# Performance work log

Measured on AMD Instinct MI355X. Metric: run time of the kernel, lower is better.

The kernel has to match this reference:

```python
import jax, jax.numpy as jnp
import numpy as np

D_MODEL = 1024
NUM_HEADS = 16


def setup_inputs() -> dict:
    key = jax.random.key(0)
    ks = jax.random.split(key, 5)
    sigma = (2.0 / (D_MODEL + D_MODEL)) ** 0.5
    def trunc(k):
        # truncated normal in [-3*sigma, 3*sigma], std sigma
        return sigma * jax.random.truncated_normal(k, -3.0, 3.0, (D_MODEL, D_MODEL), jnp.float32)
    x = jax.random.normal(ks[0], (4, 2048, D_MODEL), jnp.float32)
    return {
        "x": x,
        "W_Q": trunc(ks[1]),
        "W_K": trunc(ks[2]),
        "W_V": trunc(ks[3]),
        "W_O": trunc(ks[4]),
    }


def _mha(x, W_Q, W_K, W_V, W_O):
    B, S, D = x.shape
    H = NUM_HEADS
    dk = D // H
    # Linear stores W as (d_out, d_in); einsum '... d_in, d_out d_in -> ... d_out'
    Q = jnp.einsum('bsd,ed->bse', x, W_Q).reshape(B, S, H, dk).transpose(0, 2, 1, 3)
    K = jnp.einsum('bsd,ed->bse', x, W_K).reshape(B, S, H, dk).transpose(0, 2, 1, 3)
    V = jnp.einsum('bsd,ed->bse', x, W_V).reshape(B, S, H, dk).transpose(0, 2, 1, 3)
    scores = jnp.einsum('bhnd,bhmd->bhnm', Q, K) / jnp.sqrt(jnp.asarray(dk, x.dtype))
    causal = jnp.tril(jnp.ones((S, S), bool))
    scores = jnp.where(causal, scores, -jnp.inf)
    attn = jax.nn.softmax(scores, axis=-1)
    out = jnp.einsum('bhnm,bhmd->bhnd', attn, V)  # [B,H,S,dk]
    out = out.transpose(0, 2, 1, 3).reshape(B, S, D)
    return jnp.einsum('bsd,ed->bse', out, W_O)


def reference(x, W_Q, W_K, W_V, W_O):
    return _mha(x, W_Q, W_K, W_V, W_O)
```

## Files before the change

### kernel.cpp

```cpp
#include <hip/hip_runtime.h>
#include <hip/hip_bf16.h>
#include <stdint.h>


typedef unsigned short u16;
typedef short bf16x8 __attribute__((ext_vector_type(8)));
typedef float f32x4 __attribute__((ext_vector_type(4)));
typedef unsigned short u16x8 __attribute__((ext_vector_type(8)));
typedef unsigned int u32x4 __attribute__((ext_vector_type(4)));

#define S_LEN 2048
#define DMODEL 1024
#define NH 16

__device__ __forceinline__ u16 f2bf(float f) {
    unsigned u = __builtin_bit_cast(unsigned, f);
    unsigned r = (u + 0x7fffu + ((u >> 16) & 1u)) >> 16;
    return (u16)r;
}

__device__ __forceinline__ float fast_exp2(float x) {
    return __builtin_amdgcn_exp2f(x);
}

__device__ __forceinline__ unsigned cvtpk_bf16(float lo, float hi_) {
    unsigned r;
    asm("v_cvt_pk_bf16_f32 %0, %1, %2" : "=v"(r) : "v"(lo), "v"(hi_));
    return r;
}

__device__ __forceinline__ void pl32swap(unsigned& a, unsigned& b) {
    asm("v_permlane32_swap_b32 %0, %1" : "+v"(a), "+v"(b));
}
__device__ __forceinline__ void pl16swap(unsigned& a, unsigned& b) {
    asm("v_permlane16_swap_b32 %0, %1" : "+v"(a), "+v"(b));
}

__device__ __forceinline__ void gll16(const void* g, void* s) {
    __builtin_amdgcn_global_load_lds((const __attribute__((address_space(1))) unsigned*)g,
                                     (__attribute__((address_space(3))) unsigned*)s, 16, 0, 0);
}

__global__ __launch_bounds__(256) void cast_all(
    const float* __restrict__ x, const float* __restrict__ wq, const float* __restrict__ wk,
    const float* __restrict__ wv, const float* __restrict__ wo,
    u16* __restrict__ xb, u16* __restrict__ wqkv, u16* __restrict__ wob, int nx) {
    const int NW = DMODEL * DMODEL;
    int i4 = (blockIdx.x * 256 + threadIdx.x) * 4;
    const float* src; u16* dst; int off;
    if (i4 < nx)             { src = x;  dst = xb;            off = i4; }
    else if (i4 < nx + NW)   { src = wq; dst = wqkv;          off = i4 - nx; }
    else if (i4 < nx + 2*NW) { src = wk; dst = wqkv + NW;     off = i4 - nx - NW; }
    else if (i4 < nx + 3*NW) { src = wv; dst = wqkv + 2*NW;   off = i4 - nx - 2*NW; }
    else                     { src = wo; dst = wob;           off = i4 - nx - 3*NW; }
    float4 v = *reinterpret_cast<const float4*>(src + off);
    ushort4 o4; o4.x = f2bf(v.x); o4.y = f2bf(v.y); o4.z = f2bf(v.z); o4.w = f2bf(v.w);
    *reinterpret_cast<ushort4*>(dst + off) = o4;
}

template <typename OUT>
__global__ __launch_bounds__(256) void gemm_bt(const u16* __restrict__ A, const u16* __restrict__ B,
                                               OUT* __restrict__ C, int M, int N, int K,
                                               int qcols, float qscale, u16* __restrict__ vt) {
    __shared__ u16 As[128 * 64];
    __shared__ u16 Bs[128 * 64];
    __shared__ u16 Ts[4][16 * 72];
    const int m0 = blockIdx.y * 128, n0 = blockIdx.x * 128;
    const int t = threadIdx.x, w = t >> 6, l = t & 63;
    const int hi = l >> 4;
    const int wr = w >> 1, wc = w & 1;
    f32x4 acc[4][4] = {};

    const int lr = l >> 3;
    const int lc = l & 7;
    const int gcol = (lc ^ lr) * 8;
    const u16* Ag = A + (size_t)(m0 + w * 32 + lr) * K + gcol;
    const u16* Bg = B + (size_t)(n0 + w * 32 + lr) * K + gcol;

    for (int k0 = 0; k0 < K; k0 += 64) {
        __syncthreads();
#pragma unroll
        for (int c = 0; c < 4; c++) {
            gll16(Ag + (size_t)c * 8 * K + k0, As + w * 2048 + c * 512);
            gll16(Bg + (size_t)c * 8 * K + k0, Bs + w * 2048 + c * 512);
        }
        __syncthreads();
#pragma unroll
        for (int kk = 0; kk < 2; kk++) {
            bf16x8 af[4], bfr[4];
#pragma unroll
            for (int mi = 0; mi < 4; mi++)
                af[mi] = *(const bf16x8*)&As[(wr * 64 + mi * 16 + (l & 15)) * 64 +
                                             (((kk * 4 + hi) ^ (l & 7)) * 8)];
#pragma unroll
            for (int ni = 0; ni < 4; ni++)
                bfr[ni] = *(const bf16x8*)&Bs[(wc * 64 + ni * 16 + (l & 15)) * 64 +
                                              (((kk * 4 + hi) ^ (l & 7)) * 8)];
#pragma unroll
            for (int mi = 0; mi < 4; mi++)
#pragma unroll
                for (int ni = 0; ni < 4; ni++)
                    acc[mi][ni] = __builtin_amdgcn_mfma_f32_16x16x32_bf16(af[mi], bfr[ni], acc[mi][ni], 0, 0, 0);
        }
    }

    if (vt != nullptr && n0 >= 2048) {
        const int mw = m0 + wr * 64;
        const int bq = mw >> 11;
        const int s0w = mw & (S_LEN - 1);
        const int hd = ((n0 + wc * 64) - 2048) >> 6;
        u16* tb = &Ts[w][0];
#pragma unroll
        for (int ni = 0; ni < 4; ni++) {
#pragma unroll
            for (int mi = 0; mi < 4; mi++) {
                uint2 pk = make_uint2(cvtpk_bf16(acc[mi][ni][0], acc[mi][ni][1]),
                                      cvtpk_bf16(acc[mi][ni][2], acc[mi][ni][3]));
                *(uint2*)&tb[(l & 15) * 72 + mi * 16 + hi * 4] = pk;
            }
            bf16x8 r0 = *(const bf16x8*)&tb[(l & 15) * 72 + hi * 16];
            bf16x8 r1 = *(const bf16x8*)&tb[(l & 15) * 72 + hi * 16 + 8];
            size_t vrow = ((size_t)(bq * 16 + hd) * 64 + ni * 16 + (l & 15)) * S_LEN + s0w + hi * 16;
            *(u16x8*)&vt[vrow]     = (u16x8)r0;
            *(u16x8*)&vt[vrow + 8] = (u16x8)r1;
        }
    } else {
#pragma unroll
        for (int mi = 0; mi < 4; mi++)
#pragma unroll
            for (int ni = 0; ni < 4; ni++)
#pragma unroll
                for (int j = 0; j < 4; j++) {
                    int r = m0 + wr * 64 + mi * 16 + hi * 4 + j;
                    int c = n0 + wc * 64 + ni * 16 + (l & 15);
                    float v = acc[mi][ni][j];
                    if (c < qcols) v *= qscale;
                    if constexpr (__is_same(OUT, u16)) C[(size_t)r * N + c] = f2bf(v);
                    else                               C[(size_t)r * N + c] = v;
                }
    }
}

__global__ __launch_bounds__(256, 3) void attn(const u16* __restrict__ QKV, const u16* __restrict__ VT,
                                               u16* __restrict__ O) {
    const int bh = blockIdx.x, y = blockIdx.y;
    const int p = (y < 8) ? y : 23 - y;
    const int b = bh >> 4, h = bh & 15;
    const int t = threadIdx.x, w = t >> 6, l = t & 63;
    const int q = l & 15, hi = l >> 4, s7 = q & 7;

    __shared__ u16 SM[2][2][64][64];

    const int srow = t >> 3, sblk = t & 7;
    const int gs = (sblk ^ (srow & 7)) * 8;
    const u16* Kg = QKV + (size_t)(b * S_LEN + srow) * 3072 + 1024 + h * 64 + gs;
    const u16* Vg = VT + (size_t)(bh * 64 + srow) * S_LEN + gs;
    const u16* Kg2 = Kg + (size_t)32 * 3072;
    const u16* Vg2 = Vg + (size_t)32 * S_LEN;

    const int kA0 = q * 128 + ((hi ^ s7) << 4);
    const int kA1 = kA0 ^ 64;
    const char* smbase = (const char*)&SM[0][0][0][0];

    const int q128 = p * 128;
    const int nt = 2 * p + 2;
    const int qgA = q128 + w * 16 + q;
    const int qgB = qgA + 64;

    bf16x8 qfA[2], qfB[2];
#pragma unroll
    for (int kk = 0; kk < 2; kk++) {
        qfA[kk] = *(const bf16x8*)&QKV[(size_t)(b * S_LEN + qgA) * 3072 + h * 64 + kk * 32 + hi * 8];
        qfB[kk] = *(const bf16x8*)&QKV[(size_t)(b * S_LEN + qgB) * 3072 + h * 64 + kk * 32 + hi * 8];
    }

    f32x4 oaccA[4] = {}, oaccB[4] = {};
    float ssA = 0.f, ssB = 0.f;

    gll16(Kg,  (u16*)&SM[0][0][0][0] + t * 8);
    gll16(Kg2, (u16*)&SM[0][0][0][0] + 2048 + t * 8);
    gll16(Vg,  (u16*)&SM[0][1][0][0] + t * 8);
    gll16(Vg2, (u16*)&SM[0][1][0][0] + 2048 + t * 8);
    __syncthreads();

    const u16* KgT  = Kg  + (size_t)64 * 3072;
    const u16* Kg2T = Kg2 + (size_t)64 * 3072;
    const u16* VgT  = Vg  + 64;
    const u16* Vg2T = Vg2 + 64;

#pragma unroll 1
    for (int tt = 0; tt < nt; ++tt) {
        const int cur = tt & 1;
        if (tt + 1 < nt) {
            gll16(KgT,  (u16*)&SM[cur ^ 1][0][0][0] + t * 8);
            gll16(Kg2T, (u16*)&SM[cur ^ 1][0][0][0] + 2048 + t * 8);
            gll16(VgT,  (u16*)&SM[cur ^ 1][1][0][0] + t * 8);
            gll16(Vg2T, (u16*)&SM[cur ^ 1][1][0][0] + 2048 + t * 8);
            KgT  += (size_t)64 * 3072;
            Kg2T += (size_t)64 * 3072;
            VgT  += 64;
            Vg2T += 64;
        }
        const int kv0 = tt * 64;
        const char* kb = smbase + cur * 16384;

        f32x4 saccA[4] = {}, saccB[4] = {};
        __builtin_amdgcn_s_setprio(1);
#pragma unroll
        for (int kk = 0; kk < 2; kk++) {
            const char* ka = kb + (kk ? kA1 : kA0);
#pragma unroll
            for (int ni = 0; ni < 4; ni++) {
                bf16x8 kf = *(const bf16x8*)(ka + ni * 2048);
                saccA[ni] = __builtin_amdgcn_mfma_f32_16x16x32_bf16(kf, qfA[kk], saccA[ni], 0, 0, 0);
                saccB[ni] = __builtin_amdgcn_mfma_f32_16x16x32_bf16(kf, qfB[kk], saccB[ni], 0, 0, 0);
            }
        }
        __builtin_amdgcn_s_setprio(0);

        bf16x8 pfA0, pfA1, pfB0, pfB1;
        {
            const int r0 = qgA - kv0;
            if (r0 < 63) {
                const int rth = r0 - hi * 4;
#pragma unroll
                for (int ni = 0; ni < 4; ni++)
#pragma unroll
                    for (int j = 0; j < 4; j++)
                        if (ni * 16 + j > rth) saccA[ni][j] = -1e30f;
            }
            float pv[4][4];
#pragma unroll
            for (int ni = 0; ni < 4; ni++)
#pragma unroll
                for (int j = 0; j < 4; j++) pv[ni][j] = fast_exp2(saccA[ni][j] - 8.0f);
            ssA += ((pv[0][0] + pv[0][1]) + (pv[0][2] + pv[0][3]))
                 + ((pv[1][0] + pv[1][1]) + (pv[1][2] + pv[1][3]))
                 + ((pv[2][0] + pv[2][1]) + (pv[2][2] + pv[2][3]))
                 + ((pv[3][0] + pv[3][1]) + (pv[3][2] + pv[3][3]));
            unsigned c00 = cvtpk_bf16(pv[0][0], pv[0][1]), c01 = cvtpk_bf16(pv[0][2], pv[0][3]);
            unsigned c10 = cvtpk_bf16(pv[1][0], pv[1][1]), c11 = cvtpk_bf16(pv[1][2], pv[1][3]);
            unsigned c20 = cvtpk_bf16(pv[2][0], pv[2][1]), c21 = cvtpk_bf16(pv[2][2], pv[2][3]);
            unsigned c30 = cvtpk_bf16(pv[3][0], pv[3][1]), c31 = cvtpk_bf16(pv[3][2], pv[3][3]);
            pl32swap(c00, c10); pl16swap(c00, c10);
            pl32swap(c01, c11); pl16swap(c01, c11);
            pl32swap(c20, c30); pl16swap(c20, c30);
            pl32swap(c21, c31); pl16swap(c21, c31);
            u32x4 f0 = {c00, c01, c10, c11};
            u32x4 f1 = {c20, c21, c30, c31};
            pfA0 = __builtin_bit_cast(bf16x8, f0);
            pfA1 = __builtin_bit_cast(bf16x8, f1);
        }
        {
            const int r0 = qgB - kv0;
            if (r0 < 63) {
                const int rth = r0 - hi * 4;
#pragma unroll
                for (int ni = 0; ni < 4; ni++)
#pragma unroll
                    for (int j = 0; j < 4; j++)
                        if (ni * 16 + j > rth) saccB[ni][j] = -1e30f;
            }
            float pv[4][4];
#pragma unroll
            for (int ni = 0; ni < 4; ni++)
#pragma unroll
                for (int j = 0; j < 4; j++) pv[ni][j] = fast_exp2(saccB[ni][j] - 8.0f);
            ssB += ((pv[0][0] + pv[0][1]) + (pv[0][2] + pv[0][3]))
                 + ((pv[1][0] + pv[1][1]) + (pv[1][2] + pv[1][3]))
                 + ((pv[2][0] + pv[2][1]) + (pv[2][2] + pv[2][3]))
                 + ((pv[3][0] + pv[3][1]) + (pv[3][2] + pv[3][3]));
            unsigned c00 = cvtpk_bf16(pv[0][0], pv[0][1]), c01 = cvtpk_bf16(pv[0][2], pv[0][3]);
            unsigned c10 = cvtpk_bf16(pv[1][0], pv[1][1]), c11 = cvtpk_bf16(pv[1][2], pv[1][3]);
            unsigned c20 = cvtpk_bf16(pv[2][0], pv[2][1]), c21 = cvtpk_bf16(pv[2][2], pv[2][3]);
            unsigned c30 = cvtpk_bf16(pv[3][0], pv[3][1]), c31 = cvtpk_bf16(pv[3][2], pv[3][3]);
            pl32swap(c00, c10); pl16swap(c00, c10);
            pl32swap(c01, c11); pl16swap(c01, c11);
            pl32swap(c20, c30); pl16swap(c20, c30);
            pl32swap(c21, c31); pl16swap(c21, c31);
            u32x4 f0 = {c00, c01, c10, c11};
            u32x4 f1 = {c20, c21, c30, c31};
            pfB0 = __builtin_bit_cast(bf16x8, f0);
            pfB1 = __builtin_bit_cast(bf16x8, f1);
        }

        const char* vb = kb + 8192;
        __builtin_amdgcn_s_setprio(1);
#pragma unroll
        for (int kk = 0; kk < 2; kk++) {
            const char* va = vb + (kk ? kA1 : kA0);
            bf16x8 pfa = kk ? pfA1 : pfA0;
            bf16x8 pfb = kk ? pfB1 : pfB0;
#pragma unroll
            for (int di = 0; di < 4; di++) {
                bf16x8 vf = *(const bf16x8*)(va + di * 2048);
                oaccA[di] = __builtin_amdgcn_mfma_f32_16x16x32_bf16(vf, pfa, oaccA[di], 0, 0, 0);
                oaccB[di] = __builtin_amdgcn_mfma_f32_16x16x32_bf16(vf, pfb, oaccB[di], 0, 0, 0);
            }
        }
        __builtin_amdgcn_s_setprio(0);
        __syncthreads();
    }

    {
        float ssr = ssA;
        ssr += __shfl_xor(ssr, 16, 64);
        ssr += __shfl_xor(ssr, 32, 64);
        float inv = 1.0f / ssr;
#pragma unroll
        for (int di = 0; di < 4; di++) {
            ushort4 o4;
            o4.x = f2bf(oaccA[di][0] * inv);
            o4.y = f2bf(oaccA[di][1] * inv);
            o4.z = f2bf(oaccA[di][2] * inv);
            o4.w = f2bf(oaccA[di][3] * inv);
            *(ushort4*)&O[(size_t)(b * S_LEN + qgA) * DMODEL + h * 64 + di * 16 + hi * 4] = o4;
        }
    }
    {
        float ssr = ssB;
        ssr += __shfl_xor(ssr, 16, 64);
        ssr += __shfl_xor(ssr, 32, 64);
        float inv = 1.0f / ssr;
#pragma unroll
        for (int di = 0; di < 4; di++) {
            ushort4 o4;
            o4.x = f2bf(oaccB[di][0] * inv);
            o4.y = f2bf(oaccB[di][1] * inv);
            o4.z = f2bf(oaccB[di][2] * inv);
            o4.w = f2bf(oaccB[di][3] * inv);
            *(ushort4*)&O[(size_t)(b * S_LEN + qgB) * DMODEL + h * 64 + di * 16 + hi * 4] = o4;
        }
    }
}

extern "C" void kernel_launch(void* const* d_in, const int* in_sizes, int n_in,
                              void* d_out, int out_size, void* d_ws, size_t ws_size,
                              hipStream_t stream) {
    const float* x  = (const float*)d_in[0];
    const float* wq = (const float*)d_in[1];
    const float* wk = (const float*)d_in[2];
    const float* wv = (const float*)d_in[3];
    const float* wo = (const float*)d_in[4];
    const int nx = in_sizes[0];
    const int BS = nx / DMODEL;
    const int NW = DMODEL * DMODEL;

    u16* xb   = (u16*)d_ws;
    u16* wqkv = xb + (size_t)nx;
    u16* wob  = wqkv + (size_t)3 * NW;
    u16* qkv  = wob + (size_t)NW;
    u16* vt   = qkv + (size_t)BS * 3072;
    u16* ob   = vt + (size_t)nx;

    int ncast = (nx + 4 * NW) / 4 / 256;
    cast_all<<<ncast, 256, 0, stream>>>(x, wq, wk, wv, wo, xb, wqkv, wob, nx);

    const float QSC = 0.125f * 1.44269504088896f;
    gemm_bt<u16><<<dim3(3072 / 128, BS / 128), 256, 0, stream>>>(xb, wqkv, qkv, BS, 3072, DMODEL,
                                                                 DMODEL, QSC, vt);

    attn<<<dim3((BS / S_LEN) * NH, 16), 256, 0, stream>>>(qkv, vt, ob);

    gemm_bt<float><<<dim3(DMODEL / 128, BS / 128), 256, 0, stream>>>(ob, wob, (float*)d_out, BS, DMODEL, DMODEL,
                                                                     0, 1.0f, nullptr);
}
```

Measured before the change: 154.0 us.

## Triple-buffer K/V tiles in attention with prefetch distance two and explicit waitcnt

The attention kernel's shared-memory K/V staging moves from double to triple buffering. Two tiles are prefetched ahead, and each iteration waits on outstanding loads with s_waitcnt vmcnt(4) plus a single barrier, replacing the trailing __syncthreads. The aim is to hide global-to-LDS load latency better and remove one barrier per iteration. In exchange, LDS use per block rises from 32KB to 48KB, which may cut occupancy under launch_bounds(256,3).

```diff
diff --git a/kernel.cpp b/kernel.cpp
--- a/kernel.cpp
+++ b/kernel.cpp
@@ -149,7 +149,7 @@
     const int t = threadIdx.x, w = t >> 6, l = t & 63;
     const int q = l & 15, hi = l >> 4, s7 = q & 7;
 
-    __shared__ u16 SM[2][2][64][64];
+    __shared__ u16 SM[3][2][64][64];
 
     const int srow = t >> 3, sblk = t & 7;
     const int gs = (sblk ^ (srow & 7)) * 8;
@@ -160,7 +160,6 @@
 
     const int kA0 = q * 128 + ((hi ^ s7) << 4);
     const int kA1 = kA0 ^ 64;
-    const char* smbase = (const char*)&SM[0][0][0][0];
 
     const int q128 = p * 128;
     const int nt = 2 * p + 2;
@@ -177,32 +176,31 @@
     f32x4 oaccA[4] = {}, oaccB[4] = {};
     float ssA = 0.f, ssB = 0.f;
 
-    gll16(Kg,  (u16*)&SM[0][0][0][0] + t * 8);
-    gll16(Kg2, (u16*)&SM[0][0][0][0] + 2048 + t * 8);
-    gll16(Vg,  (u16*)&SM[0][1][0][0] + t * 8);
-    gll16(Vg2, (u16*)&SM[0][1][0][0] + 2048 + t * 8);
-    __syncthreads();
-
-    const u16* KgT  = Kg  + (size_t)64 * 3072;
-    const u16* Kg2T = Kg2 + (size_t)64 * 3072;
-    const u16* VgT  = Vg  + 64;
-    const u16* Vg2T = Vg2 + 64;
+    gll16(Kg,                       (u16*)&SM[0][0][0][0] + t * 8);
+    gll16(Kg2,                      (u16*)&SM[0][0][0][0] + 2048 + t * 8);
+    gll16(Vg,                       (u16*)&SM[0][1][0][0] + t * 8);
+    gll16(Vg2,                      (u16*)&SM[0][1][0][0] + 2048 + t * 8);
+    gll16(Kg  + (size_t)64 * 3072,  (u16*)&SM[1][0][0][0] + t * 8);
+    gll16(Kg2 + (size_t)64 * 3072,  (u16*)&SM[1][0][0][0] + 2048 + t * 8);
+    gll16(Vg  + 64,                 (u16*)&SM[1][1][0][0] + t * 8);
+    gll16(Vg2 + 64,                 (u16*)&SM[1][1][0][0] + 2048 + t * 8);
 
 #pragma unroll 1
     for (int tt = 0; tt < nt; ++tt) {
-        const int cur = tt & 1;
-        if (tt + 1 < nt) {
-            gll16(KgT,  (u16*)&SM[cur ^ 1][0][0][0] + t * 8);
-            gll16(Kg2T, (u16*)&SM[cur ^ 1][0][0][0] + 2048 + t * 8);
-            gll16(VgT,  (u16*)&SM[cur ^ 1][1][0][0] + t * 8);
-            gll16(Vg2T, (u16*)&SM[cur ^ 1][1][0][0] + 2048 + t * 8);
-            KgT  += (size_t)64 * 3072;
-            Kg2T += (size_t)64 * 3072;
-            VgT  += 64;
-            Vg2T += 64;
+        const int cur = tt % 3;
+        if (tt + 1 < nt) { asm volatile("s_waitcnt vmcnt(4)" ::: "memory"); }
+        else             { asm volatile("s_waitcnt vmcnt(0)" ::: "memory"); }
+        __builtin_amdgcn_s_barrier();
+        if (tt + 2 < nt) {
+            const int nb = (tt + 2) % 3;
+            const size_t koff = (size_t)(tt + 2) * 64;
+            gll16(Kg  + koff * 3072, (u16*)&SM[nb][0][0][0] + t * 8);
+            gll16(Kg2 + koff * 3072, (u16*)&SM[nb][0][0][0] + 2048 + t * 8);
+            gll16(Vg  + koff,        (u16*)&SM[nb][1][0][0] + t * 8);
+            gll16(Vg2 + koff,        (u16*)&SM[nb][1][0][0] + 2048 + t * 8);
         }
         const int kv0 = tt * 64;
-        const char* kb = smbase + cur * 16384;
+        const char* kb = (const char*)&SM[cur][0][0][0];
 
         f32x4 saccA[4] = {}, saccB[4] = {};
         __builtin_amdgcn_s_setprio(1);
@@ -299,7 +297,6 @@
             }
         }
         __builtin_amdgcn_s_setprio(0);
-        __syncthreads();
     }
 
     {
```

Measured after the change: 156.4 us. No clear change (+1.6%).
